# Kernel tuning notes

Hardware: AMD Instinct MI355X
Metric: run time of the kernel (lower is better)

Reference implementation:

```python
import jax, jax.numpy as jnp
import numpy as np

T = 2048      # total tokens (single prefill sequence)
HID = 2048    # hidden_size
H = 16        # num k-heads == num v-heads
DK = 128      # key head dim
DV = 128      # value head dim
K = 4         # causal conv kernel width
EPS = 1e-6


def setup_inputs() -> dict:
    key = jax.random.key(0)
    ks = jax.random.split(key, 10)
    n = lambda k, shape, sc: (jax.random.normal(k, shape, jnp.float32) * sc)
    return {
        "hidden_states": n(ks[0], (T, HID), 1.0),
        "Wq": n(ks[1], (HID, H * DK), 0.02),
        "Wk": n(ks[2], (HID, H * DK), 0.02),
        "Wv": n(ks[3], (HID, H * DV), 0.02),
        "Wb": n(ks[4], (HID, H), 0.02),
        "conv_wq": n(ks[5], (H * DK, K), 0.5),
        "conv_wk": n(ks[6], (H * DK, K), 0.5),
        "conv_wv": n(ks[7], (H * DV, K), 0.5),
        "o_norm_w": jnp.ones((DV,), jnp.float32),
        "Wo": n(ks[8], (HID, HID), 0.02),
    }


def _causal_conv_silu(x, w):
    # x: [T, D], w: [D, K] depthwise causal conv, then SiLU (matches causal_conv1d_fn)
    xp = jnp.pad(x, ((K - 1, 0), (0, 0)))
    y = sum(xp[j:j + T] * w[:, j] for j in range(K))
    return jax.nn.silu(y)


def _l2norm(x):
    return x * jax.lax.rsqrt(jnp.sum(x * x, axis=-1, keepdims=True) + EPS)


def reference(hidden_states, Wq, Wk, Wv, Wb, conv_wq, conv_wk, conv_wv, o_norm_w, Wo):
    # projections [T, H*D]
    q = _causal_conv_silu(hidden_states @ Wq, conv_wq).reshape(T, H, DK)
    k = _causal_conv_silu(hidden_states @ Wk, conv_wk).reshape(T, H, DK)
    v = _causal_conv_silu(hidden_states @ Wv, conv_wv).reshape(T, H, DV)
    beta = jax.nn.sigmoid(hidden_states @ Wb)  # [T, H]

    # qk l2-norm + scale (FLA chunk_delta_rule defaults)
    q = _l2norm(q) * (DK ** -0.5)
    k = _l2norm(k)

    # delta-rule recurrence: S <- S + beta * k (v - k^T S)
    def step(S, inp):
        q_t, k_t, v_t, b_t = inp            # [H,DK],[H,DK],[H,DV],[H]
        kS = jnp.einsum('hk,hkv->hv', k_t, S)
        delta = b_t[:, None] * (v_t - kS)   # [H, DV]
        S = S + jnp.einsum('hk,hv->hkv', k_t, delta)
        o_t = jnp.einsum('hk,hkv->hv', q_t, S)
        return S, o_t

    S0 = jnp.zeros((H, DK, DV), jnp.float32)
    _, o = jax.lax.scan(step, S0, (q, k, v, beta))  # o: [T, H, DV]

    # per-head RMSNorm on value head dim
    o = o * jax.lax.rsqrt(jnp.mean(o * o, axis=-1, keepdims=True) + EPS) * o_norm_w
    out = o.reshape(T, H * DV) @ Wo
    return out
```

## Files before the change

### kernel.cpp

```cpp
#include <hip/hip_runtime.h>

typedef unsigned short u16;
typedef __attribute__((ext_vector_type(4))) unsigned short u16x4;
typedef __attribute__((ext_vector_type(8))) unsigned short u16x8;
typedef __attribute__((ext_vector_type(8))) short short8;
typedef __attribute__((ext_vector_type(4))) float f32x4;

#define DEVI __device__ __forceinline__

DEVI u16 f2b(float f) {
  union { float f; unsigned u; } x; x.f = f;
  unsigned r = (x.u + 0x7fffu + ((x.u >> 16) & 1u)) >> 16;
  return (u16)r;
}
DEVI float b2f(u16 h) {
  union { unsigned u; float f; } x; x.u = ((unsigned)h) << 16;
  return x.f;
}
DEVI f32x4 mfma_bf16(short8 a, short8 b, f32x4 c) {
  return __builtin_amdgcn_mfma_f32_16x16x32_bf16(a, b, c, 0, 0, 0);
}
DEVI void gl2lds16(const u16* g, u16* l) {
  __builtin_amdgcn_global_load_lds((__attribute__((address_space(1))) void*)g,
                                   (__attribute__((address_space(3))) void*)l,
                                   16, 0, 0);
}
DEVI void barrier_lds() {
  asm volatile("s_waitcnt lgkmcnt(0)\n\ts_barrier" ::: "memory");
}

__global__ void k_cvt(const float* __restrict__ src, u16* __restrict__ dst, int n4,
                      const float* __restrict__ Wb, u16* __restrict__ WbT) {
  int b = blockIdx.x;
  if (b < 4096) {
    int i = b * 256 + threadIdx.x;
    if (i < n4) {
      float4 v = ((const float4*)src)[i];
      u16x4 r; r.x = f2b(v.x); r.y = f2b(v.y); r.z = f2b(v.z); r.w = f2b(v.w);
      ((u16x4*)dst)[i] = r;
    }
  } else {
    int j = (b - 4096) * 256 + threadIdx.x;
    int n = j >> 11, k = j & 2047;
    WbT[j] = f2b(Wb[k * 16 + n]);
  }
}

__global__ __launch_bounds__(256)
void k_transpose4(const float* __restrict__ s0, const float* __restrict__ s1,
                  const float* __restrict__ s2, const float* __restrict__ s3,
                  u16* __restrict__ d0, u16* __restrict__ d1,
                  u16* __restrict__ d2, u16* __restrict__ d3) {
  const int RC = 2048;
  const float* src = (blockIdx.z == 0) ? s0 : (blockIdx.z == 1) ? s1 : (blockIdx.z == 2) ? s2 : s3;
  u16* dst = (blockIdx.z == 0) ? d0 : (blockIdx.z == 1) ? d1 : (blockIdx.z == 2) ? d2 : d3;
  __shared__ u16 tile[64 * 66];
  int bx = blockIdx.x << 6, by = blockIdx.y << 6;
  int x = threadIdx.x & 63, g = threadIdx.x >> 6;
#pragma unroll
  for (int i = 0; i < 16; ++i) {
    int r = (i << 2) + g;
    tile[x * 66 + r] = f2b(src[(size_t)(by + r) * RC + bx + x]);
  }
  __syncthreads();
#pragma unroll
  for (int i = 0; i < 16; ++i) {
    int r = (i << 2) + g;
    dst[(size_t)(bx + r) * RC + by + x] = tile[r * 66 + x];
  }
}


struct StageCtx { size_t go[2]; int lo[2]; };

DEVI void stage_half(const u16* g, const StageCtx& sc, u16* l) {
  gl2lds16(g + sc.go[0], l + sc.lo[0]);
  gl2lds16(g + sc.go[1], l + sc.lo[1]);
}

template <int MODE>
DEVI void ktile8(const u16* gA0, const u16* gA1, const u16* gB0, const u16* gB1,
                 const StageCtx& sc, u16* lds, int u,
                 const int (&aoff)[4][2], const int (&boff)[2][2],
                 f32x4 (&acc)[8][4]) {
  const int sl = (u & 1) << 13, sl1 = ((u + 1) & 1) << 13;
  const u16* hA0 = lds + sl;
  const u16* hA1 = lds + 16384 + sl;
  const u16* hB0 = lds + 32768 + sl;
  const u16* hB1 = lds + 49152 + sl;
  const size_t uo1 = (size_t)(u + 1) << 6, uo2 = (size_t)(u + 2) << 6;
  short8 a[4][2], b0[2][2], b1[2][2];
#pragma unroll
  for (int m = 0; m < 4; ++m) {
    a[m][0] = *(const short8*)(hA0 + aoff[m][0]);
    a[m][1] = *(const short8*)(hA0 + aoff[m][1]);
  }
#pragma unroll
  for (int n = 0; n < 2; ++n) {
    b0[n][0] = *(const short8*)(hB0 + boff[n][0]);
    b0[n][1] = *(const short8*)(hB0 + boff[n][1]);
  }
  if constexpr (MODE <= 1) stage_half(gA1 + uo1, sc, lds + 16384 + sl1);
  __builtin_amdgcn_s_barrier();
  asm volatile("s_waitcnt lgkmcnt(0)" ::: "memory");
  __builtin_amdgcn_s_setprio(1);
#pragma unroll
  for (int m = 0; m < 4; ++m)
#pragma unroll
    for (int n = 0; n < 2; ++n) {
      acc[m][n] = mfma_bf16(a[m][0], b0[n][0], acc[m][n]);
      acc[m][n] = mfma_bf16(a[m][1], b0[n][1], acc[m][n]);
    }
  __builtin_amdgcn_s_setprio(0);
  __builtin_amdgcn_s_barrier();
#pragma unroll
  for (int n = 0; n < 2; ++n) {
    b1[n][0] = *(const short8*)(hB1 + boff[n][0]);
    b1[n][1] = *(const short8*)(hB1 + boff[n][1]);
  }
  if constexpr (MODE == 0) stage_half(gA0 + uo2, sc, lds + sl);
  __builtin_amdgcn_s_barrier();
  asm volatile("s_waitcnt lgkmcnt(0)" ::: "memory");
  __builtin_amdgcn_s_setprio(1);
#pragma unroll
  for (int m = 0; m < 4; ++m)
#pragma unroll
    for (int n = 0; n < 2; ++n) {
      acc[m][2 + n] = mfma_bf16(a[m][0], b1[n][0], acc[m][2 + n]);
      acc[m][2 + n] = mfma_bf16(a[m][1], b1[n][1], acc[m][2 + n]);
    }
  __builtin_amdgcn_s_setprio(0);
  __builtin_amdgcn_s_barrier();
#pragma unroll
  for (int m = 0; m < 4; ++m) {
    a[m][0] = *(const short8*)(hA1 + aoff[m][0]);
    a[m][1] = *(const short8*)(hA1 + aoff[m][1]);
  }
  if constexpr (MODE == 0) stage_half(gB0 + uo2, sc, lds + 32768 + sl);
  __builtin_amdgcn_s_barrier();
  asm volatile("s_waitcnt lgkmcnt(0)" ::: "memory");
  __builtin_amdgcn_s_setprio(1);
#pragma unroll
  for (int m = 0; m < 4; ++m)
#pragma unroll
    for (int n = 0; n < 2; ++n) {
      acc[4 + m][n] = mfma_bf16(a[m][0], b0[n][0], acc[4 + m][n]);
      acc[4 + m][n] = mfma_bf16(a[m][1], b0[n][1], acc[4 + m][n]);
    }
  __builtin_amdgcn_s_setprio(0);
  __builtin_amdgcn_s_barrier();
  if constexpr (MODE == 0) stage_half(gB1 + uo2, sc, lds + 49152 + sl);
  __builtin_amdgcn_s_barrier();
  __builtin_amdgcn_s_setprio(1);
#pragma unroll
  for (int m = 0; m < 4; ++m)
#pragma unroll
    for (int n = 0; n < 2; ++n) {
      acc[4 + m][2 + n] = mfma_bf16(a[m][0], b1[n][0], acc[4 + m][2 + n]);
      acc[4 + m][2 + n] = mfma_bf16(a[m][1], b1[n][1], acc[4 + m][2 + n]);
    }
  __builtin_amdgcn_s_setprio(0);
  if constexpr (MODE == 0) asm volatile("s_waitcnt vmcnt(6)" ::: "memory");
  if constexpr (MODE == 1) asm volatile("s_waitcnt vmcnt(0)" ::: "memory");
  __builtin_amdgcn_s_barrier();
}

__global__ __launch_bounds__(512, 2)
void k_gemm8p(const u16* __restrict__ A, const u16* __restrict__ BT,
              u16* __restrict__ Cb, int N, int K) {
  __shared__ __align__(16) u16 lds[65536];
  const int tid = threadIdx.x, wave = tid >> 6, lane = tid & 63;
  const int wm = wave >> 2, wn = wave & 3;
  const int fr = lane & 15, fq = (lane >> 4) << 4;
  const long bm = (long)blockIdx.y << 8, bn = (long)blockIdx.x << 8;
  const int NT = K >> 6;
  int aoff[4][2], boff[2][2];
#pragma unroll
  for (int m = 0; m < 4; ++m)
#pragma unroll
    for (int ks = 0; ks < 2; ++ks) {
      int row = (wm << 6) + (m << 4) + fr;
      int kb = (ks << 6) + fq;
      aoff[m][ks] = (row << 6) + ((kb ^ ((fr & 7) << 4)) >> 1);
    }
#pragma unroll
  for (int n = 0; n < 2; ++n)
#pragma unroll
    for (int ks = 0; ks < 2; ++ks) {
      int row = (wn << 5) + (n << 4) + fr;
      int kb = (ks << 6) + fq;
      boff[n][ks] = (row << 6) + ((kb ^ ((fr & 7) << 4)) >> 1);
    }
  StageCtx sc;
#pragma unroll
  for (int s = 0; s < 2; ++s) {
    int c = (s << 9) + tid, row = c >> 3;
    int kbs = (((c & 7) << 4) ^ ((row & 7) << 4));
    sc.go[s] = (size_t)row * K + (kbs >> 1);
    sc.lo[s] = ((s << 9) + (tid & ~63)) << 3;
  }
  const u16* gA0 = A + (size_t)bm * K;
  const u16* gA1 = gA0 + (size_t)128 * K;
  const u16* gB0 = BT + (size_t)bn * K;
  const u16* gB1 = gB0 + (size_t)128 * K;
  f32x4 acc[8][4];
#pragma unroll
  for (int i = 0; i < 8; ++i)
#pragma unroll
    for (int j = 0; j < 4; ++j) acc[i][j] = (f32x4){0.f, 0.f, 0.f, 0.f};
  stage_half(gA0, sc, lds + 0);
  stage_half(gA1, sc, lds + 16384);
  stage_half(gB0, sc, lds + 32768);
  stage_half(gB1, sc, lds + 49152);
  asm volatile("s_waitcnt vmcnt(4)" ::: "memory");
  stage_half(gA0 + 64, sc, lds + 8192);
  stage_half(gB0 + 64, sc, lds + 40960);
  stage_half(gB1 + 64, sc, lds + 57344);
  asm volatile("s_waitcnt vmcnt(6)" ::: "memory");
  __builtin_amdgcn_s_barrier();
  for (int u = 0; u + 2 < NT; ++u)
    ktile8<0>(gA0, gA1, gB0, gB1, sc, lds, u, aoff, boff, acc);
  ktile8<1>(gA0, gA1, gB0, gB1, sc, lds, NT - 2, aoff, boff, acc);
  ktile8<2>(gA0, gA1, gB0, gB1, sc, lds, NT - 1, aoff, boff, acc);
  const int er = (lane >> 4) << 2, ec = lane & 15;
#pragma unroll
  for (int ai = 0; ai < 8; ++ai) {
    long row0 = bm + ((long)(ai >> 2) << 7) + (wm << 6) + ((ai & 3) << 4) + er;
#pragma unroll
    for (int bj = 0; bj < 4; ++bj) {
      long col = bn + ((long)(bj >> 1) << 7) + (wn << 5) + ((bj & 1) << 4) + ec;
#pragma unroll
      for (int r = 0; r < 4; ++r)
        Cb[(size_t)(row0 + r) * N + col] = f2b(acc[ai][bj][r]);
    }
  }
}

__global__ __launch_bounds__(256, 4)
void k_gemm_wo(const u16* __restrict__ A, const u16* __restrict__ BT,
               float* __restrict__ Cf, int M, int N, int K) {
  __shared__ __align__(16) u16 As[2048];
  __shared__ __align__(16) u16 Bs[2048];
  const int tid = threadIdx.x, wave = tid >> 6, lane = tid & 63;
  const long bm = (long)blockIdx.y << 6, bn = (long)blockIdx.x << 6;
  const int r0 = (wave << 4) + (lane >> 2);
  const int kof = (((lane & 3) ^ ((lane >> 3) & 3)) << 3);
  const u16* gA = A + (bm + r0) * (long)K + kof;
  const u16* gB = BT + (bn + r0) * (long)K + kof;
  u16* lA = As + (wave << 9);
  u16* lB = Bs + (wave << 9);
  const int wr = (wave >> 1) << 5, wc = (wave & 1) << 5;
  const int fr = lane & 15, fq = (lane >> 4) << 3;
  const int fqs = fq ^ (((fr >> 1) & 3) << 3);
  f32x4 acc[2][2];
#pragma unroll
  for (int i = 0; i < 2; ++i)
#pragma unroll
    for (int j = 0; j < 2; ++j) acc[i][j] = (f32x4){0.f, 0.f, 0.f, 0.f};
  for (int k0 = 0; k0 < K; k0 += 32) {
    gl2lds16(gA + k0, lA);
    gl2lds16(gB + k0, lB);
    __syncthreads();
    short8 af[2], bfr[2];
#pragma unroll
    for (int t = 0; t < 2; ++t) {
      af[t]  = *(const short8*)&As[(wr + (t << 4) + fr) * 32 + fqs];
      bfr[t] = *(const short8*)&Bs[(wc + (t << 4) + fr) * 32 + fqs];
    }
#pragma unroll
    for (int i = 0; i < 2; ++i)
#pragma unroll
      for (int j = 0; j < 2; ++j)
        acc[i][j] = mfma_bf16(af[i], bfr[j], acc[i][j]);
    __syncthreads();
  }
  const int er = (lane >> 4) << 2, ec = lane & 15;
#pragma unroll
  for (int i = 0; i < 2; ++i)
#pragma unroll
    for (int j = 0; j < 2; ++j)
#pragma unroll
      for (int r = 0; r < 4; ++r) {
        long row = bm + wr + (i << 4) + er + r;
        long col = bn + wc + (j << 4) + ec;
        Cf[row * N + col] = acc[i][j][r];
      }
}

__global__ __launch_bounds__(256, 4)
void k_beta(const u16* __restrict__ Xb, const u16* __restrict__ WbT,
            float* __restrict__ beta) {
  __shared__ float part[4][256];
  int tid = threadIdx.x, w = tid >> 6, lane = tid & 63;
  int t0 = blockIdx.x << 4;
  int fr = lane & 15, fq = (lane >> 4) << 3;
  const u16* ap = Xb + (size_t)(t0 + fr) * 2048 + (w << 9) + fq;
  const u16* bp = WbT + (size_t)fr * 2048 + (w << 9) + fq;
  f32x4 acc = {0.f, 0.f, 0.f, 0.f};
#pragma unroll
  for (int ks = 0; ks < 16; ++ks)
    acc = mfma_bf16(*(const short8*)(ap + (ks << 5)), *(const short8*)(bp + (ks << 5)), acc);
  int er = (lane >> 4) << 2;
#pragma unroll
  for (int r = 0; r < 4; ++r) part[w][(er + r) * 16 + fr] = acc[r];
  __syncthreads();
  float s = part[0][tid] + part[1][tid] + part[2][tid] + part[3][tid];
  beta[(t0 << 4) + tid] = 1.f / (1.f + __expf(-s));
}

__global__ __launch_bounds__(256, 4)
void k_conv(const u16* __restrict__ qkv,
            const float* __restrict__ cwq, const float* __restrict__ cwk,
            const float* __restrict__ cwv,
            u16* __restrict__ qn, u16* __restrict__ kn, u16* __restrict__ vn) {
  __shared__ __align__(16) u16 xs[67 * 136];
  __shared__ float wf[128 * 4];
  int tt = blockIdx.x, s = blockIdx.y;
  int kind = s >> 4, h = s & 15;
  int t0 = tt << 6;
  int col = (kind << 11) + (h << 7);
  int tid = threadIdx.x;
  const float* cw = (kind == 0) ? cwq : ((kind == 1) ? cwk : cwv);
  if (tid < 128) *(float4*)&wf[tid << 2] = *(const float4*)(cw + (size_t)((h << 7) + tid) * 4);
  for (int i = tid; i < 1072; i += 256) {
    int prow = i >> 4, c8 = (i & 15) << 3;
    int g = t0 - 3 + prow;
    u16x8 v = {0, 0, 0, 0, 0, 0, 0, 0};
    if (g >= 0) v = *(const u16x8*)(qkv + (size_t)g * 6144 + col + c8);
    *(u16x8*)&xs[prow * 136 + c8] = v;
  }
  __syncthreads();
  int t = tid >> 2, dg = tid & 3;
  float y[32];
  float ss = 0.f;
#pragma unroll
  for (int e8 = 0; e8 < 4; ++e8) {
    int d0 = (dg << 5) + (e8 << 3);
    u16x8 a0 = *(const u16x8*)&xs[(t + 0) * 136 + d0];
    u16x8 a1 = *(const u16x8*)&xs[(t + 1) * 136 + d0];
    u16x8 a2 = *(const u16x8*)&xs[(t + 2) * 136 + d0];
    u16x8 a3 = *(const u16x8*)&xs[(t + 3) * 136 + d0];
#pragma unroll
    for (int e = 0; e < 8; ++e) {
      float4 w = *(const float4*)&wf[(d0 + e) << 2];
      float v = b2f(a0[e]) * w.x + b2f(a1[e]) * w.y + b2f(a2[e]) * w.z + b2f(a3[e]) * w.w;
      v = v / (1.f + __expf(-v));
      y[(e8 << 3) + e] = v;
      ss += v * v;
    }
  }
  float sc = 1.f;
  if (kind < 2) {
    ss += __shfl_xor(ss, 1);
    ss += __shfl_xor(ss, 2);
    sc = rsqrtf(ss + 1e-6f);
    if (kind == 0) sc *= 0.08838834764831843f;
  }
  u16* dst = (kind == 0) ? qn : ((kind == 1) ? kn : vn);
  u16* dp = dst + ((size_t)h << 18) + ((size_t)(t0 + t) << 7) + (dg << 5);
#pragma unroll
  for (int e8 = 0; e8 < 4; ++e8) {
    u16x8 p;
#pragma unroll
    for (int e = 0; e < 8; ++e) p[e] = f2b(y[(e8 << 3) + e] * sc);
    *(u16x8*)(dp + (e8 << 3)) = p;
  }
}

__global__ __launch_bounds__(256, 2)
void k_prep(const u16* __restrict__ qn, const u16* __restrict__ kn, const u16* __restrict__ vn,
            const float* __restrict__ beta,
            u16* __restrict__ Gg, u16* __restrict__ Wg,
            u16* __restrict__ KTg, u16* __restrict__ UTg) {
  __shared__ __align__(16) char sm[70912];
  u16*  Kc  = (u16*)sm;
  u16*  Qc  = (u16*)(sm + 17408);
  u16*  Vc  = (u16*)(sm + 34816);
  u16*  KTl = (u16*)(sm + 52224);
  float* AL = (float*)(sm + 52224);
  float* Bl = (float*)(sm + 70656);
  u16*  WR  = Qc;
  int h = blockIdx.x, c = blockIdx.y;
  int tid = threadIdx.x, wave = tid >> 6, lane = tid & 63;
  size_t ch = (size_t)(c * 16 + h);
  const u16* kb = kn + ((size_t)h << 18) + ((size_t)c << 13);
  const u16* qb = qn + ((size_t)h << 18) + ((size_t)c << 13);
  const u16* vb = vn + ((size_t)h << 18) + ((size_t)c << 13);
#pragma unroll
  for (int s = 0; s < 4; ++s) {
    int e = (tid + (s << 8)) << 3;
    int t = e >> 7, d = e & 127;
    *(u16x8*)&Kc[t * 136 + d] = *(const u16x8*)(kb + e);
    *(u16x8*)&Qc[t * 136 + d] = *(const u16x8*)(qb + e);
    *(u16x8*)&Vc[t * 136 + d] = *(const u16x8*)(vb + e);
  }
  if (tid < 64) Bl[tid] = beta[((c << 6) + tid) * 16 + h];
  __syncthreads();
  int fr = lane & 15, fq = (lane >> 4) << 3, q4 = (lane >> 4) << 2;
  int arow = (wave << 4) + fr;
  f32x4 kk[4], qk[4];
#pragma unroll
  for (int ct = 0; ct < 4; ++ct) { kk[ct] = (f32x4){0.f,0.f,0.f,0.f}; qk[ct] = (f32x4){0.f,0.f,0.f,0.f}; }
#pragma unroll
  for (int ks = 0; ks < 4; ++ks) {
    short8 aK = *(const short8*)&Kc[arow * 136 + (ks << 5) + fq];
    short8 aQ = *(const short8*)&Qc[arow * 136 + (ks << 5) + fq];
#pragma unroll
    for (int ct = 0; ct < 4; ++ct) {
      short8 bK = *(const short8*)&Kc[((ct << 4) + fr) * 136 + (ks << 5) + fq];
      kk[ct] = mfma_bf16(aK, bK, kk[ct]);
      qk[ct] = mfma_bf16(aQ, bK, qk[ct]);
    }
  }
#pragma unroll
  for (int ct = 0; ct < 4; ++ct)
#pragma unroll
    for (int r = 0; r < 4; ++r) {
      int i = (wave << 4) + q4 + r, j = (ct << 4) + fr;
      Gg[(ch << 12) + i * 64 + j] = f2b((j <= i) ? qk[ct][r] : 0.f);
    }
  {
    int d = tid & 127, tg = tid >> 7;
#pragma unroll
    for (int it = 0; it < 4; ++it) {
      int t0 = (tg + (it << 1)) << 3;
      u16x8 pk;
#pragma unroll
      for (int j = 0; j < 8; ++j) pk[j] = Kc[(t0 + j) * 136 + d];
      *(u16x8*)&KTl[d * 72 + t0] = pk;
    }
  }
  __syncthreads();
#pragma unroll
  for (int it = 0; it < 4; ++it) {
    int idx = tid + (it << 8);
    int row = idx >> 3, j8 = (idx & 7) << 3;
    *(u16x8*)(KTg + (ch << 13) + (row << 6) + j8) = *(const u16x8*)&KTl[row * 72 + j8];
  }
  __syncthreads();
  {
    float bi[4];
#pragma unroll
    for (int r = 0; r < 4; ++r) bi[r] = Bl[(wave << 4) + q4 + r];
#pragma unroll
    for (int ct = 0; ct < 4; ++ct)
#pragma unroll
      for (int r = 0; r < 4; ++r) {
        int i = (wave << 4) + q4 + r, j = (ct << 4) + fr;
        AL[i * 64 + j] = (j < i) ? bi[r] * kk[ct][r] : 0.f;
      }
  }
  __syncthreads();
  float X[64];
  {
    const u16* colp = (tid < 128) ? (Kc + tid) : (Vc + (tid - 128));
#pragma unroll
    for (int t = 0; t < 64; ++t) X[t] = Bl[t] * b2f(colp[t * 136]);
#pragma unroll
    for (int r = 1; r < 64; ++r) {
      float s = 0.f;
      const float* Ar = &AL[r * 64];
      int r4 = r & ~3;
#pragma unroll
      for (int l = 0; l < 64; l += 4)
        if (l + 4 <= r) {
          float4 a = *(const float4*)(Ar + l);
          s += a.x * X[l] + a.y * X[l + 1] + a.z * X[l + 2] + a.w * X[l + 3];
        }
#pragma unroll
      for (int l = 0; l < 4; ++l)
        if (r4 + l < r) s += Ar[r4 + l] * X[r4 + l];
      X[r] -= s;
    }
  }
  __syncthreads();
  if (tid < 128) {
#pragma unroll
    for (int t = 0; t < 64; ++t) WR[t * 136 + tid] = f2b(X[t]);
  } else {
    int v = tid - 128;
    u16* dstr = UTg + (ch << 13) + (v << 6);
#pragma unroll
    for (int j = 0; j < 8; ++j) {
      u16x8 p;
#pragma unroll
      for (int e = 0; e < 8; ++e) p[e] = f2b(X[(j << 3) + e]);
      *(u16x8*)(dstr + (j << 3)) = p;
    }
  }
  __syncthreads();
#pragma unroll
  for (int it = 0; it < 4; ++it) {
    int idx = tid + (it << 8);
    int row = idx >> 4, j8 = (idx & 15) << 3;
    *(u16x8*)(Wg + (ch << 13) + (row << 7) + j8) = *(const u16x8*)&WR[row * 136 + j8];
  }
}

struct Frags { short8 q[4], w[4], g[2], k[4]; u16x4 u; };

DEVI void load_frags(Frags& f, const u16* qh, const u16* Wg, const u16* Gg,
                     const u16* KTg, const u16* UTg, int c, int h,
                     int trow, int fr, int fq, int q4, int w, int vbase) {
  const u16* qb = qh + ((size_t)((c << 6) + trow + fr) << 7) + fq;
#pragma unroll
  for (int ks = 0; ks < 4; ++ks) f.q[ks] = *(const short8*)(qb + (ks << 5));
  size_t ch = (size_t)(c * 16 + h);
  const u16* wb = Wg + (ch << 13) + ((size_t)(trow + fr) << 7) + fq;
#pragma unroll
  for (int ks = 0; ks < 4; ++ks) f.w[ks] = *(const short8*)(wb + (ks << 5));
  const u16* gb = Gg + (ch << 12) + ((size_t)(trow + fr) << 6) + fq;
#pragma unroll
  for (int ks = 0; ks < 2; ++ks) f.g[ks] = *(const short8*)(gb + (ks << 5));
  const u16* kbp = KTg + (ch << 13) + ((size_t)(w << 5) << 6) + fq;
#pragma unroll
  for (int dt = 0; dt < 2; ++dt)
#pragma unroll
    for (int ks = 0; ks < 2; ++ks)
      f.k[(dt << 1) | ks] = *(const short8*)(kbp + ((size_t)((dt << 4) + fr) << 6) + (ks << 5));
  f.u = *(const u16x4*)(UTg + (ch << 13) + ((size_t)(vbase + fr) << 6) + trow + q4);
}

DEVI void chunk_body(int c, Frags& f, u16* ST, u16* DT, u16* oh,
                     int trow, int fr, int fq, int q4, int w, int vbase,
                     f32x4& S0, f32x4& S1) {
#pragma unroll
  for (int r = 0; r < 4; ++r) {
    ST[(q4 + r) * 136 + (w << 5) + fr] = f2b(S0[r]);
    ST[(q4 + r) * 136 + (w << 5) + 16 + fr] = f2b(S1[r]);
  }
  barrier_lds();
  short8 sf[4];
#pragma unroll
  for (int ks = 0; ks < 4; ++ks) sf[ks] = *(const short8*)&ST[fr * 136 + (ks << 5) + fq];
  f32x4 racc = {0.f,0.f,0.f,0.f}, oacc = {0.f,0.f,0.f,0.f};
#pragma unroll
  for (int ks = 0; ks < 4; ++ks) {
    racc = mfma_bf16(f.w[ks], sf[ks], racc);
    oacc = mfma_bf16(f.q[ks], sf[ks], oacc);
  }
#pragma unroll
  for (int r = 0; r < 4; ++r)
    DT[fr * 72 + trow + q4 + r] = f2b(b2f(f.u[r]) - racc[r]);
  barrier_lds();
  short8 df[2];
#pragma unroll
  for (int ks = 0; ks < 2; ++ks) df[ks] = *(const short8*)&DT[fr * 72 + (ks << 5) + fq];
#pragma unroll
  for (int ks = 0; ks < 2; ++ks) {
    oacc = mfma_bf16(f.g[ks], df[ks], oacc);
    S0 = mfma_bf16(df[ks], f.k[ks], S0);
    S1 = mfma_bf16(df[ks], f.k[2 | ks], S1);
  }
#pragma unroll
  for (int r = 0; r < 4; ++r)
    oh[(size_t)((c << 6) + trow + q4 + r) * 128 + vbase + fr] = f2b(oacc[r]);
}

__global__ __launch_bounds__(256, 1)
void k_delta(const u16* __restrict__ qn, const u16* __restrict__ Wg,
             const u16* __restrict__ Gg, const u16* __restrict__ KTg,
             const u16* __restrict__ UTg, u16* __restrict__ o) {
  __shared__ __align__(16) u16 ST[16 * 136];
  __shared__ __align__(16) u16 DT[16 * 72];
  int bx = blockIdx.x;
  int h = bx & 15, vbase = (bx >> 4) << 4;
  int tid = threadIdx.x, w = tid >> 6, lane = tid & 63;
  int fr = lane & 15, fq = (lane >> 4) << 3, q4 = (lane >> 4) << 2;
  int trow = w << 4;
  const u16* qh = qn + ((size_t)h << 18);
  u16* oh = o + ((size_t)h << 18);
  f32x4 S0 = {0.f,0.f,0.f,0.f}, S1 = {0.f,0.f,0.f,0.f};
  Frags fa, fb;
  load_frags(fa, qh, Wg, Gg, KTg, UTg, 0, h, trow, fr, fq, q4, w, vbase);
  for (int c = 0; c < 32; c += 2) {
    int c1 = c + 1, c2 = (c + 2 < 32) ? c + 2 : 31;
    load_frags(fb, qh, Wg, Gg, KTg, UTg, c1, h, trow, fr, fq, q4, w, vbase);
    chunk_body(c, fa, ST, DT, oh, trow, fr, fq, q4, w, vbase, S0, S1);
    load_frags(fa, qh, Wg, Gg, KTg, UTg, c2, h, trow, fr, fq, q4, w, vbase);
    chunk_body(c1, fb, ST, DT, oh, trow, fr, fq, q4, w, vbase, S0, S1);
  }
}

__global__ __launch_bounds__(256, 4)
void k_onorm(const u16* __restrict__ o, const float* __restrict__ onw,
             u16* __restrict__ onb) {
  __shared__ float wl[128];
  int tt = blockIdx.x, h = blockIdx.y, tid = threadIdx.x;
  if (tid < 128) wl[tid] = onw[tid];
  __syncthreads();
  int t = tid >> 2, dg = tid & 3;
  const u16* src = o + ((size_t)h << 18) + ((size_t)((tt << 6) + t) << 7) + (dg << 5);
  u16x8 a[4];
  float ss = 0.f;
#pragma unroll
  for (int e8 = 0; e8 < 4; ++e8) {
    a[e8] = *(const u16x8*)(src + (e8 << 3));
#pragma unroll
    for (int e = 0; e < 8; ++e) { float x = b2f(a[e8][e]); ss += x * x; }
  }
  ss += __shfl_xor(ss, 1);
  ss += __shfl_xor(ss, 2);
  float inv = rsqrtf(ss * (1.f / 128.f) + 1e-6f);
  u16* dp = onb + ((size_t)((tt << 6) + t) << 11) + (h << 7) + (dg << 5);
#pragma unroll
  for (int e8 = 0; e8 < 4; ++e8) {
    u16x8 p;
#pragma unroll
    for (int e = 0; e < 8; ++e)
      p[e] = f2b(b2f(a[e8][e]) * inv * wl[(dg << 5) + (e8 << 3) + e]);
    *(u16x8*)(dp + (e8 << 3)) = p;
  }
}

extern "C" void kernel_launch(void* const* d_in, const int* in_sizes, int n_in,
                              void* d_out, int out_size, void* d_ws, size_t ws_size,
                              hipStream_t stream) {
  (void)in_sizes; (void)n_in; (void)out_size; (void)ws_size;
  const float* hs  = (const float*)d_in[0];
  const float* Wq  = (const float*)d_in[1];
  const float* Wk  = (const float*)d_in[2];
  const float* Wv  = (const float*)d_in[3];
  const float* Wb  = (const float*)d_in[4];
  const float* cwq = (const float*)d_in[5];
  const float* cwk = (const float*)d_in[6];
  const float* cwv = (const float*)d_in[7];
  const float* onw = (const float*)d_in[8];
  const float* Wo  = (const float*)d_in[9];
  float* out = (float*)d_out;
  char* ws = (char*)d_ws;
  const size_t MB = 1ull << 20;
  u16*  Xb   = (u16*)(ws);
  u16*  WT   = (u16*)(ws + 8  * MB);
  u16*  WoT  = (u16*)(ws + 32 * MB);
  u16*  QKV  = (u16*)(ws + 40 * MB);
  u16*  Wg   = (u16*)(ws + 40 * MB);
  u16*  KTg  = (u16*)(ws + 48 * MB);
  u16*  UTg  = (u16*)(ws + 56 * MB);
  u16*  qn_  = (u16*)(ws + 64 * MB);
  u16*  kn_  = (u16*)(ws + 72 * MB);
  u16*  vn_  = (u16*)(ws + 80 * MB);
  float* beta= (float*)(ws + 88 * MB);
  u16*  WbT  = (u16*)(ws + 88 * MB + 512 * 1024);
  u16*  Gm   = (u16*)(ws + 89 * MB);
  u16*  o_   = (u16*)(ws + 93 * MB);
  u16*  onb  = (u16*)(ws + 109 * MB);

  k_cvt<<<4224, 256, 0, stream>>>(hs, Xb, 2048 * 2048 / 4, Wb, WbT);
  k_transpose4<<<dim3(32, 32, 4), 256, 0, stream>>>(
      Wq, Wk, Wv, Wo, WT, WT + 2048 * 2048, WT + 2 * 2048 * 2048, WoT);
  k_gemm8p<<<dim3(24, 8), 512, 0, stream>>>(Xb, WT, QKV, 6144, 2048);
  k_beta<<<128, 256, 0, stream>>>(Xb, WbT, beta);
  k_conv<<<dim3(32, 48), 256, 0, stream>>>(QKV, cwq, cwk, cwv, qn_, kn_, vn_);
  k_prep<<<dim3(16, 32), 256, 0, stream>>>(qn_, kn_, vn_, beta, Gm, Wg, KTg, UTg);
  k_delta<<<128, 256, 0, stream>>>(qn_, Wg, Gm, KTg, UTg, o_);
  k_onorm<<<dim3(32, 16), 256, 0, stream>>>(o_, onw, onb);
  k_gemm_wo<<<dim3(32, 32), 256, 0, stream>>>(onb, WoT, out, 2048, 2048, 2048);
}
```

Measured before the change: 340.7 us.

## Software-pipeline LDS fragment reads across MFMA quadrants in projection GEMM

Restructures the 256x256 bf16 GEMM inner loop so LDS reads of the next A/B fragments are issued before the current quadrant's MFMAs instead of waiting on lgkmcnt(0) first. Fragments now live in persistent double register sets (a0/a1/b0/b1), and the next k-tile's A0/B0 are preloaded at the end of each iteration. This cuts barriers and explicit LDS waits per k-tile, so LDS latency overlaps with matrix math. The cost is higher register pressure, more reliance on compiler-inserted waits, and a retuned vmcnt schedule that must still guarantee staged data has landed.

```diff
diff --git a/kernel.cpp b/kernel.cpp
--- a/kernel.cpp
+++ b/kernel.cpp
@@ -78,91 +78,68 @@
   gl2lds16(g + sc.go[1], l + sc.lo[1]);
 }
 
+DEVI void rdA(const u16* h, const int (&aoff)[4][2], short8 (&a)[4][2]) {
+#pragma unroll
+  for (int m = 0; m < 4; ++m) {
+    a[m][0] = *(const short8*)(h + aoff[m][0]);
+    a[m][1] = *(const short8*)(h + aoff[m][1]);
+  }
+}
+DEVI void rdB(const u16* h, const int (&boff)[2][2], short8 (&b)[2][2]) {
+#pragma unroll
+  for (int n = 0; n < 2; ++n) {
+    b[n][0] = *(const short8*)(h + boff[n][0]);
+    b[n][1] = *(const short8*)(h + boff[n][1]);
+  }
+}
+
+template <int QA, int QB>
+DEVI void mmquad(const short8 (&a)[4][2], const short8 (&b)[2][2], f32x4 (&acc)[8][4]) {
+  __builtin_amdgcn_s_setprio(1);
+#pragma unroll
+  for (int m = 0; m < 4; ++m)
+#pragma unroll
+    for (int n = 0; n < 2; ++n) {
+      acc[(QA << 2) + m][(QB << 1) + n] =
+          mfma_bf16(a[m][0], b[n][0], acc[(QA << 2) + m][(QB << 1) + n]);
+      acc[(QA << 2) + m][(QB << 1) + n] =
+          mfma_bf16(a[m][1], b[n][1], acc[(QA << 2) + m][(QB << 1) + n]);
+    }
+  __builtin_amdgcn_s_setprio(0);
+}
+
 template <int MODE>
-DEVI void ktile8(const u16* gA0, const u16* gA1, const u16* gB0, const u16* gB1,
-                 const StageCtx& sc, u16* lds, int u,
-                 const int (&aoff)[4][2], const int (&boff)[2][2],
-                 f32x4 (&acc)[8][4]) {
-  const int sl = (u & 1) << 13, sl1 = ((u + 1) & 1) << 13;
-  const u16* hA0 = lds + sl;
-  const u16* hA1 = lds + 16384 + sl;
-  const u16* hB0 = lds + 32768 + sl;
-  const u16* hB1 = lds + 49152 + sl;
+DEVI void ktile(u16* lds, int u,
+                const u16* gA0, const u16* gA1, const u16* gB0, const u16* gB1,
+                const StageCtx& sc,
+                const int (&aoff)[4][2], const int (&boff)[2][2],
+                short8 (&a0)[4][2], short8 (&a1)[4][2],
+                short8 (&b0)[2][2], short8 (&b1)[2][2],
+                f32x4 (&acc)[8][4]) {
+  const int cs = (u & 1) << 13, ns = ((u + 1) & 1) << 13;
+  const u16* A1c = lds + 16384 + cs;
+  const u16* B1c = lds + 49152 + cs;
   const size_t uo1 = (size_t)(u + 1) << 6, uo2 = (size_t)(u + 2) << 6;
-  short8 a[4][2], b0[2][2], b1[2][2];
-#pragma unroll
-  for (int m = 0; m < 4; ++m) {
-    a[m][0] = *(const short8*)(hA0 + aoff[m][0]);
-    a[m][1] = *(const short8*)(hA0 + aoff[m][1]);
-  }
-#pragma unroll
-  for (int n = 0; n < 2; ++n) {
-    b0[n][0] = *(const short8*)(hB0 + boff[n][0]);
-    b0[n][1] = *(const short8*)(hB0 + boff[n][1]);
-  }
-  if constexpr (MODE <= 1) stage_half(gA1 + uo1, sc, lds + 16384 + sl1);
   __builtin_amdgcn_s_barrier();
-  asm volatile("s_waitcnt lgkmcnt(0)" ::: "memory");
-  __builtin_amdgcn_s_setprio(1);
-#pragma unroll
-  for (int m = 0; m < 4; ++m)
-#pragma unroll
-    for (int n = 0; n < 2; ++n) {
-      acc[m][n] = mfma_bf16(a[m][0], b0[n][0], acc[m][n]);
-      acc[m][n] = mfma_bf16(a[m][1], b0[n][1], acc[m][n]);
-    }
-  __builtin_amdgcn_s_setprio(0);
+  rdB(B1c, boff, b1);
+  if constexpr (MODE <= 1) stage_half(gA1 + uo1, sc, lds + 16384 + ns);
+  mmquad<0, 0>(a0, b0, acc);
   __builtin_amdgcn_s_barrier();
-#pragma unroll
-  for (int n = 0; n < 2; ++n) {
-    b1[n][0] = *(const short8*)(hB1 + boff[n][0]);
-    b1[n][1] = *(const short8*)(hB1 + boff[n][1]);
-  }
-  if constexpr (MODE == 0) stage_half(gA0 + uo2, sc, lds + sl);
+  rdA(A1c, aoff, a1);
+  if constexpr (MODE == 0) stage_half(gA0 + uo2, sc, lds + cs);
+  mmquad<0, 1>(a0, b1, acc);
   __builtin_amdgcn_s_barrier();
-  asm volatile("s_waitcnt lgkmcnt(0)" ::: "memory");
-  __builtin_amdgcn_s_setprio(1);
-#pragma unroll
-  for (int m = 0; m < 4; ++m)
-#pragma unroll
-    for (int n = 0; n < 2; ++n) {
-      acc[m][2 + n] = mfma_bf16(a[m][0], b1[n][0], acc[m][2 + n]);
-      acc[m][2 + n] = mfma_bf16(a[m][1], b1[n][1], acc[m][2 + n]);
-    }
-  __builtin_amdgcn_s_setprio(0);
-  __builtin_amdgcn_s_barrier();
-#pragma unroll
-  for (int m = 0; m < 4; ++m) {
-    a[m][0] = *(const short8*)(hA1 + aoff[m][0]);
-    a[m][1] = *(const short8*)(hA1 + aoff[m][1]);
-  }
-  if constexpr (MODE == 0) stage_half(gB0 + uo2, sc, lds + 32768 + sl);
-  __builtin_amdgcn_s_barrier();
-  asm volatile("s_waitcnt lgkmcnt(0)" ::: "memory");
-  __builtin_amdgcn_s_setprio(1);
-#pragma unroll
-  for (int m = 0; m < 4; ++m)
-#pragma unroll
-    for (int n = 0; n < 2; ++n) {
-      acc[4 + m][n] = mfma_bf16(a[m][0], b0[n][0], acc[4 + m][n]);
-      acc[4 + m][n] = mfma_bf16(a[m][1], b0[n][1], acc[4 + m][n]);
-    }
-  __builtin_amdgcn_s_setprio(0);
-  __builtin_amdgcn_s_barrier();
-  if constexpr (MODE == 0) stage_half(gB1 + uo2, sc, lds + 49152 + sl);
-  __builtin_amdgcn_s_barrier();
-  __builtin_amdgcn_s_setprio(1);
-#pragma unroll
-  for (int m = 0; m < 4; ++m)
-#pragma unroll
-    for (int n = 0; n < 2; ++n) {
-      acc[4 + m][2 + n] = mfma_bf16(a[m][0], b1[n][0], acc[4 + m][2 + n]);
-      acc[4 + m][2 + n] = mfma_bf16(a[m][1], b1[n][1], acc[4 + m][2 + n]);
-    }
-  __builtin_amdgcn_s_setprio(0);
-  if constexpr (MODE == 0) asm volatile("s_waitcnt vmcnt(6)" ::: "memory");
+  if constexpr (MODE == 0) stage_half(gB0 + uo2, sc, lds + 32768 + cs);
+  mmquad<1, 0>(a1, b0, acc);
+  if constexpr (MODE == 0) asm volatile("s_waitcnt vmcnt(4)" ::: "memory");
   if constexpr (MODE == 1) asm volatile("s_waitcnt vmcnt(0)" ::: "memory");
   __builtin_amdgcn_s_barrier();
+  if constexpr (MODE <= 1) {
+    rdA(lds + ns, aoff, a0);
+    rdB(lds + 32768 + ns, boff, b0);
+  }
+  if constexpr (MODE == 0) stage_half(gB1 + uo2, sc, lds + 49152 + cs);
+  mmquad<1, 1>(a1, b1, acc);
 }
 
 __global__ __launch_bounds__(512, 2)
@@ -208,20 +185,22 @@
   for (int i = 0; i < 8; ++i)
 #pragma unroll
     for (int j = 0; j < 4; ++j) acc[i][j] = (f32x4){0.f, 0.f, 0.f, 0.f};
+  short8 a0[4][2], a1[4][2], b0[2][2], b1[2][2];
   stage_half(gA0, sc, lds + 0);
   stage_half(gA1, sc, lds + 16384);
   stage_half(gB0, sc, lds + 32768);
   stage_half(gB1, sc, lds + 49152);
-  asm volatile("s_waitcnt vmcnt(4)" ::: "memory");
   stage_half(gA0 + 64, sc, lds + 8192);
-  stage_half(gB0 + 64, sc, lds + 40960);
-  stage_half(gB1 + 64, sc, lds + 57344);
+  stage_half(gB0 + 64, sc, lds + 32768 + 8192);
+  stage_half(gB1 + 64, sc, lds + 49152 + 8192);
   asm volatile("s_waitcnt vmcnt(6)" ::: "memory");
   __builtin_amdgcn_s_barrier();
+  rdA(lds + 0, aoff, a0);
+  rdB(lds + 32768, boff, b0);
   for (int u = 0; u + 2 < NT; ++u)
-    ktile8<0>(gA0, gA1, gB0, gB1, sc, lds, u, aoff, boff, acc);
-  ktile8<1>(gA0, gA1, gB0, gB1, sc, lds, NT - 2, aoff, boff, acc);
-  ktile8<2>(gA0, gA1, gB0, gB1, sc, lds, NT - 1, aoff, boff, acc);
+    ktile<0>(lds, u, gA0, gA1, gB0, gB1, sc, aoff, boff, a0, a1, b0, b1, acc);
+  ktile<1>(lds, NT - 2, gA0, gA1, gB0, gB1, sc, aoff, boff, a0, a1, b0, b1, acc);
+  ktile<2>(lds, NT - 1, gA0, gA1, gB0, gB1, sc, aoff, boff, a0, a1, b0, b1, acc);
   const int er = (lane >> 4) << 2, ec = lane & 15;
 #pragma unroll
   for (int ai = 0; ai < 8; ++ai) {
```

After: 335.3 us. No clear change (-1.6%).
